# Kernel tuning notes

Measured on AMD Instinct MI355X. Metric: run time of the kernel, lower is better.

## Reference

```python
import jax, jax.numpy as jnp
import numpy as np

N, E = 50000, 800000
DIN, DOUT, DIM, K = 64, 64, 3, 8
EPS_GMM = 1e-15
BN_EPS = 1e-5
ALPHA = 0.01


def setup_inputs() -> dict:
    key = jax.random.key(0)
    ks = jax.random.split(key, 10)
    x = jax.random.normal(ks[0], (N, DIN), dtype=jnp.float32)
    edge_idx = jax.random.randint(ks[1], (2, E), 0, N, dtype=jnp.int64)
    edge_attr = jax.random.uniform(ks[2], (E, DIM), dtype=jnp.float32)
    # GMMConv params (PyG: g maps in -> K*out, lin is root weight, plus bias)
    W_g = jax.random.normal(ks[3], (DIN, K * DOUT), dtype=jnp.float32) * (1.0 / np.sqrt(DIN))
    mu = jax.random.normal(ks[4], (K, DIM), dtype=jnp.float32)
    sigma = jnp.ones((K, DIM), dtype=jnp.float32) + 0.1 * jax.random.normal(ks[5], (K, DIM), dtype=jnp.float32)
    W_root = jax.random.normal(ks[6], (DIN, DOUT), dtype=jnp.float32) * (1.0 / np.sqrt(DIN))
    bias = jnp.zeros((DOUT,), dtype=jnp.float32)
    gamma = jnp.ones((DOUT,), dtype=jnp.float32)
    beta = jnp.zeros((DOUT,), dtype=jnp.float32)
    return {"x": x, "edge_idx": edge_idx, "edge_attr": edge_attr,
            "W_g": W_g, "mu": mu, "sigma": sigma, "W_root": W_root,
            "bias": bias, "gamma": gamma, "beta": beta}


def reference(x, edge_idx, edge_attr, W_g, mu, sigma, W_root, bias, gamma, beta):
    src, dst = edge_idx[0], edge_idx[1]
    # Gaussian mixture edge weights: [E, K]
    diff = edge_attr[:, None, :] - mu[None, :, :]              # [E, K, DIM]
    gauss = jnp.exp((-0.5 * diff * diff / (EPS_GMM + sigma[None] ** 2)).sum(-1))  # [E, K]
    # Transform node features once: [N, K, DOUT]
    x_trans = (x @ W_g).reshape(N, K, DOUT)
    # Per-edge message: weighted sum over kernels of gathered source features
    msg = jnp.einsum('ekm,ek->em', x_trans[src], gauss)        # [E, DOUT]
    # Mean-aggregate to destination nodes
    agg = jax.ops.segment_sum(msg, dst, num_segments=N)        # [N, DOUT]
    cnt = jax.ops.segment_sum(jnp.ones((E,), dtype=x.dtype), dst, num_segments=N)
    agg = agg / jnp.maximum(cnt, 1.0)[:, None]
    # Root weight + bias
    out = agg + x @ W_root + bias
    # BatchNorm1d (training mode: batch stats, biased variance)
    m = out.mean(axis=0)
    v = ((out - m) ** 2).mean(axis=0)
    out = gamma * (out - m) * jax.lax.rsqrt(v + BN_EPS) + beta
    # LeakyReLU
    return jnp.where(out > 0, out, ALPHA * out)
```

## Files before the change

kernel.cpp:

```cpp
#include <hip/hip_runtime.h>
#include <hip/hip_bf16.h>

#define N_NODES 50000
#define N_EDGES 800000
#define NB 391
#define BCAP 2560

typedef __hip_bfloat16 bf16;

__device__ __forceinline__ float bf_lo(int u) { union { int i; float f; } c; c.i = (unsigned)u << 16; return c.f; }
__device__ __forceinline__ float bf_hi(int u) { union { int i; float f; } c; c.i = (unsigned)u & 0xffff0000u; return c.f; }
__device__ __forceinline__ unsigned short bfbits(float f) {
    bf16 b = __float2bfloat16(f);
    union { bf16 b; unsigned short u; } c; c.b = b; return c.u;
}

__global__ void gemm_xt_kernel(const float* __restrict__ x, const float* __restrict__ Wg,
                               bf16* __restrict__ xt) {
    __shared__ float xs[16][64];
    __shared__ float lb[16 * 512];
    const int tid = threadIdx.x;
    const int row0 = blockIdx.x << 4;
    for (int i = tid; i < 1024; i += 256) xs[i >> 6][i & 63] = x[(size_t)row0 * 64 + i];
    __syncthreads();

    float a0[16], a1[16];
#pragma unroll
    for (int r = 0; r < 16; r++) { a0[r] = 0.f; a1[r] = 0.f; }
#pragma unroll 4
    for (int i = 0; i < 64; i++) {
        const float w0 = Wg[i * 512 + tid];
        const float w1 = Wg[i * 512 + tid + 256];
#pragma unroll
        for (int r = 0; r < 16; r++) {
            const float xv = xs[r][i];
            a0[r] = fmaf(xv, w0, a0[r]);
            a1[r] = fmaf(xv, w1, a1[r]);
        }
    }
#pragma unroll
    for (int r = 0; r < 16; r++) {
        lb[r * 512 + tid] = a0[r];
        lb[r * 512 + tid + 256] = a1[r];
    }
    __syncthreads();

    const int m = tid & 63, rg = tid >> 6;
#pragma unroll
    for (int rr = 0; rr < 4; rr++) {
        const int r = rg * 4 + rr;
        unsigned short h[8];
#pragma unroll
        for (int k = 0; k < 8; k++) h[k] = bfbits(lb[r * 512 + k * 64 + m]);
        int4 q;
        q.x = (int)h[0] | ((int)h[1] << 16);
        q.y = (int)h[2] | ((int)h[3] << 16);
        q.z = (int)h[4] | ((int)h[5] << 16);
        q.w = (int)h[6] | ((int)h[7] << 16);
        ((int4*)(xt + (size_t)(row0 + r) * 512))[m] = q;
    }
}

__global__ void __launch_bounds__(1024) scatter_kernel(const int* __restrict__ eidx,
                                                       const float* __restrict__ eattr,
                                                       const float* __restrict__ mu,
                                                       const float* __restrict__ sigma,
                                                       int* __restrict__ cursor,
                                                       unsigned* __restrict__ meta,
                                                       int4* __restrict__ g8v) {
    __shared__ float smu[24], sc1[24];
    __shared__ int cnt[NB], base[NB];
    const int tid = threadIdx.x;
    if (tid < 24) {
        smu[tid] = mu[tid];
        const float s = sigma[tid];
        sc1[tid] = -0.5f / (s * s + 1e-15f);
    }
    if (tid < NB) cnt[tid] = 0;
    __syncthreads();

    const int e = blockIdx.x * 1024 + tid;
    const bool act = e < N_EDGES;
    int b = 0, rank = 0;
    unsigned mt = 0;
    int4 q = {0, 0, 0, 0};
    if (act) {
        const int src = eidx[e];
        const int dst = eidx[N_EDGES + e];
        const float A0 = eattr[3 * e + 0];
        const float A1 = eattr[3 * e + 1];
        const float A2 = eattr[3 * e + 2];
        unsigned short h[8];
#pragma unroll
        for (int k = 0; k < 8; k++) {
            const float d0 = A0 - smu[3 * k + 0];
            const float d1 = A1 - smu[3 * k + 1];
            const float d2 = A2 - smu[3 * k + 2];
            const float g = __expf(fmaf(d0 * d0, sc1[3 * k + 0],
                                   fmaf(d1 * d1, sc1[3 * k + 1],
                                        d2 * d2 * sc1[3 * k + 2])));
            h[k] = bfbits(g);
        }
        q.x = (int)h[0] | ((int)h[1] << 16);
        q.y = (int)h[2] | ((int)h[3] << 16);
        q.z = (int)h[4] | ((int)h[5] << 16);
        q.w = (int)h[6] | ((int)h[7] << 16);
        b = dst >> 7;
        mt = (unsigned)src | ((unsigned)(dst & 127) << 16);
        rank = atomicAdd(&cnt[b], 1);
    }
    __syncthreads();
    if (tid < NB) {
        const int c = cnt[tid];
        base[tid] = c ? atomicAdd(&cursor[tid], c) : 0;
    }
    __syncthreads();
    if (act) {
        const int slot = b * BCAP + base[b] + rank;
        meta[slot] = mt;
        g8v[slot] = q;
    }
}

__global__ void __launch_bounds__(1024) agg_kernel(const int* __restrict__ cursor,
                                                   const unsigned* __restrict__ meta,
                                                   const int4* __restrict__ g8v,
                                                   const bf16* __restrict__ xt,
                                                   const float* __restrict__ x,
                                                   const float* __restrict__ Wr,
                                                   const float* __restrict__ bias,
                                                   float* __restrict__ out,
                                                   double* __restrict__ colsum,
                                                   double* __restrict__ colsumsq) {
    __shared__ float acc[128 * 64];
    __shared__ float wr[4096];
    __shared__ int cnt[128];
    __shared__ float red[16 * 64];

    const int tid = threadIdx.x;
    const int b = blockIdx.x;
    for (int i = tid; i < 8192; i += 1024) acc[i] = 0.f;
    if (tid < 128) cnt[tid] = 0;
    for (int i = tid; i < 4096; i += 1024) wr[i] = Wr[i];
    __syncthreads();

    int count = cursor[b];
    if (count > BCAP) count = BCAP;
    const int wid = tid >> 6, lane = tid & 63;
    const int baseSlot = b * BCAP;

    for (int j = wid; j < count; j += 16) {
        const unsigned mt = meta[baseSlot + j];
        const int4 g = g8v[baseSlot + j];
        const int src = mt & 0xffff;
        const int dl = (mt >> 16) & 127;
        const int4 qx = *(const int4*)(xt + (size_t)src * 512 + lane * 8);
        const float v = bf_lo(g.x) * bf_lo(qx.x) + bf_hi(g.x) * bf_hi(qx.x)
                      + bf_lo(g.y) * bf_lo(qx.y) + bf_hi(g.y) * bf_hi(qx.y)
                      + bf_lo(g.z) * bf_lo(qx.z) + bf_hi(g.z) * bf_hi(qx.z)
                      + bf_lo(g.w) * bf_lo(qx.w) + bf_hi(g.w) * bf_hi(qx.w);
        atomicAdd(&acc[dl * 64 + lane], v);
        if (lane == 0) atomicAdd(&cnt[dl], 1);
    }
    __syncthreads();

    const float bsv = bias[lane];
    float s = 0.f, sq = 0.f;
#pragma unroll
    for (int t = 0; t < 8; t++) {
        const int nl = wid * 8 + t;
        const int n = b * 128 + nl;
        if (n < N_NODES) {
            const float* xr = x + (size_t)n * 64;
            float a = 0.f;
#pragma unroll
            for (int i = 0; i < 64; i++) a = fmaf(xr[i], wr[i * 64 + lane], a);
            const float c = (float)cnt[nl];
            const float val = acc[nl * 64 + lane] / fmaxf(c, 1.f) + a + bsv;
            out[(size_t)n * 64 + lane] = val;
            s += val;
            sq += val * val;
        }
    }
    red[wid * 64 + lane] = s;
    __syncthreads();
    float ts = 0.f;
    if (wid == 0) {
#pragma unroll
        for (int w = 0; w < 16; w++) ts += red[w * 64 + lane];
    }
    __syncthreads();
    red[wid * 64 + lane] = sq;
    __syncthreads();
    if (wid == 0) {
        float tq = 0.f;
#pragma unroll
        for (int w = 0; w < 16; w++) tq += red[w * 64 + lane];
        atomicAdd(&colsum[lane], (double)ts);
        atomicAdd(&colsumsq[lane], (double)tq);
    }
}

__global__ void bn_prep_kernel(const double* __restrict__ colsum, const double* __restrict__ colsumsq,
                               float* __restrict__ meanr) {
    const int c = threadIdx.x;
    if (c < 64) {
        const double m = colsum[c] / (double)N_NODES;
        const double var = colsumsq[c] / (double)N_NODES - m * m;
        meanr[c] = (float)m;
        meanr[64 + c] = (float)(1.0 / sqrt(var + 1e-5));
    }
}

__global__ void finalize_kernel(float* __restrict__ out, const float* __restrict__ meanr,
                                const float* __restrict__ gamma, const float* __restrict__ beta) {
    const int i = blockIdx.x * 256 + threadIdx.x;
    const int c = i & 63;
    const float v = out[i];
    const float o = fmaf((v - meanr[c]) * meanr[64 + c], gamma[c], beta[c]);
    out[i] = o > 0.f ? o : 0.01f * o;
}

extern "C" void kernel_launch(void* const* d_in, const int* in_sizes, int n_in,
                              void* d_out, int out_size, void* d_ws, size_t ws_size,
                              hipStream_t stream) {
    const float* x     = (const float*)d_in[0];
    const int*   eidx  = (const int*)d_in[1];
    const float* eattr = (const float*)d_in[2];
    const float* Wg    = (const float*)d_in[3];
    const float* mu    = (const float*)d_in[4];
    const float* sigma = (const float*)d_in[5];
    const float* Wr    = (const float*)d_in[6];
    const float* bias  = (const float*)d_in[7];
    const float* gamma = (const float*)d_in[8];
    const float* beta  = (const float*)d_in[9];
    float* out = (float*)d_out;

    char* ws = (char*)d_ws;
    const size_t cursor_off   = 0;
    const size_t colsum_off   = 2048;
    const size_t colsumsq_off = 2560;
    const size_t zero_bytes   = 3072;
    const size_t meanr_off    = 3072;
    const size_t meta_off     = 3584;
    const size_t g8_off       = 4017664;
    const size_t xt_off       = 20073984;

    int*      cursor   = (int*)(ws + cursor_off);
    double*   colsum   = (double*)(ws + colsum_off);
    double*   colsumsq = (double*)(ws + colsumsq_off);
    float*    meanr    = (float*)(ws + meanr_off);
    unsigned* meta     = (unsigned*)(ws + meta_off);
    int4*     g8v      = (int4*)(ws + g8_off);
    bf16*     xt       = (bf16*)(ws + xt_off);

    hipMemsetAsync(ws, 0, zero_bytes, stream);
    gemm_xt_kernel<<<N_NODES / 16, 256, 0, stream>>>(x, Wg, xt);
    scatter_kernel<<<(N_EDGES + 1023) / 1024, 1024, 0, stream>>>(eidx, eattr, mu, sigma, cursor, meta, g8v);
    agg_kernel<<<NB, 1024, 0, stream>>>(cursor, meta, g8v, xt, x, Wr, bias, out, colsum, colsumsq);
    bn_prep_kernel<<<1, 64, 0, stream>>>(colsum, colsumsq, meanr);
    finalize_kernel<<<(N_NODES * 64) / 256, 256, 0, stream>>>(out, meanr, gamma, beta);
}
```

Before: 587.6 us.

## Use smaller 32-node destination buckets with batched gathers in aggregation

Destination buckets shrink from 128 to 32 nodes, so there are 1563 aggregation blocks of 256 threads in place of 391 blocks of 1024, giving better load spread across CUs. Each wave now loads 64 edge metadata entries at once and broadcasts them by shuffle, issuing four independent source-row gathers before accumulating. The root-weight matmul stages x rows in shared memory and reads Wr from global/cache in place of a shared copy. Bucket capacity drops to 704 with an overflow guard, which risks silently dropping edges if any bucket receives more.

```diff
diff --git a/kernel.cpp b/kernel.cpp
--- a/kernel.cpp
+++ b/kernel.cpp
@@ -3,8 +3,8 @@
 
 #define N_NODES 50000
 #define N_EDGES 800000
-#define NB 391
-#define BCAP 2560
+#define NB 1563
+#define BCAP 704
 
 typedef __hip_bfloat16 bf16;
 
@@ -13,6 +13,12 @@
 __device__ __forceinline__ unsigned short bfbits(float f) {
     bf16 b = __float2bfloat16(f);
     union { bf16 b; unsigned short u; } c; c.b = b; return c.u;
+}
+__device__ __forceinline__ float dot8(const int4 g, const int4 qx) {
+    return bf_lo(g.x) * bf_lo(qx.x) + bf_hi(g.x) * bf_hi(qx.x)
+         + bf_lo(g.y) * bf_lo(qx.y) + bf_hi(g.y) * bf_hi(qx.y)
+         + bf_lo(g.z) * bf_lo(qx.z) + bf_hi(g.z) * bf_hi(qx.z)
+         + bf_lo(g.w) * bf_lo(qx.w) + bf_hi(g.w) * bf_hi(qx.w);
 }
 
 __global__ void gemm_xt_kernel(const float* __restrict__ x, const float* __restrict__ Wg,
@@ -76,7 +82,7 @@
         const float s = sigma[tid];
         sc1[tid] = -0.5f / (s * s + 1e-15f);
     }
-    if (tid < NB) cnt[tid] = 0;
+    for (int i = tid; i < NB; i += 1024) cnt[i] = 0;
     __syncthreads();
 
     const int e = blockIdx.x * 1024 + tid;
@@ -105,62 +111,86 @@
         q.y = (int)h[2] | ((int)h[3] << 16);
         q.z = (int)h[4] | ((int)h[5] << 16);
         q.w = (int)h[6] | ((int)h[7] << 16);
-        b = dst >> 7;
-        mt = (unsigned)src | ((unsigned)(dst & 127) << 16);
+        b = dst >> 5;
+        mt = (unsigned)src | ((unsigned)(dst & 31) << 16);
         rank = atomicAdd(&cnt[b], 1);
     }
     __syncthreads();
-    if (tid < NB) {
-        const int c = cnt[tid];
-        base[tid] = c ? atomicAdd(&cursor[tid], c) : 0;
+    for (int i = tid; i < NB; i += 1024) {
+        const int c = cnt[i];
+        base[i] = c ? atomicAdd(&cursor[i], c) : 0;
     }
     __syncthreads();
     if (act) {
         const int slot = b * BCAP + base[b] + rank;
-        meta[slot] = mt;
-        g8v[slot] = q;
-    }
-}
-
-__global__ void __launch_bounds__(1024) agg_kernel(const int* __restrict__ cursor,
-                                                   const unsigned* __restrict__ meta,
-                                                   const int4* __restrict__ g8v,
-                                                   const bf16* __restrict__ xt,
-                                                   const float* __restrict__ x,
-                                                   const float* __restrict__ Wr,
-                                                   const float* __restrict__ bias,
-                                                   float* __restrict__ out,
-                                                   double* __restrict__ colsum,
-                                                   double* __restrict__ colsumsq) {
-    __shared__ float acc[128 * 64];
-    __shared__ float wr[4096];
-    __shared__ int cnt[128];
-    __shared__ float red[16 * 64];
+        if (slot < (b + 1) * BCAP) {
+            meta[slot] = mt;
+            g8v[slot] = q;
+        }
+    }
+}
+
+__global__ void __launch_bounds__(256) agg_kernel(const int* __restrict__ cursor,
+                                                  const unsigned* __restrict__ meta,
+                                                  const int4* __restrict__ g8v,
+                                                  const bf16* __restrict__ xt,
+                                                  const float* __restrict__ x,
+                                                  const float* __restrict__ Wr,
+                                                  const float* __restrict__ bias,
+                                                  float* __restrict__ out,
+                                                  double* __restrict__ colsum,
+                                                  double* __restrict__ colsumsq) {
+    __shared__ float acc[32 * 64];
+    __shared__ float xs[32 * 64];
+    __shared__ int cnt_s[32];
+    __shared__ float red[4 * 64];
 
     const int tid = threadIdx.x;
     const int b = blockIdx.x;
-    for (int i = tid; i < 8192; i += 1024) acc[i] = 0.f;
-    if (tid < 128) cnt[tid] = 0;
-    for (int i = tid; i < 4096; i += 1024) wr[i] = Wr[i];
+    for (int i = tid; i < 2048; i += 256) acc[i] = 0.f;
+    if (tid < 32) cnt_s[tid] = 0;
     __syncthreads();
 
     int count = cursor[b];
     if (count > BCAP) count = BCAP;
     const int wid = tid >> 6, lane = tid & 63;
-    const int baseSlot = b * BCAP;
-
-    for (int j = wid; j < count; j += 16) {
-        const unsigned mt = meta[baseSlot + j];
-        const int4 g = g8v[baseSlot + j];
-        const int src = mt & 0xffff;
-        const int dl = (mt >> 16) & 127;
-        const int4 qx = *(const int4*)(xt + (size_t)src * 512 + lane * 8);
-        const float v = bf_lo(g.x) * bf_lo(qx.x) + bf_hi(g.x) * bf_hi(qx.x)
-                      + bf_lo(g.y) * bf_lo(qx.y) + bf_hi(g.y) * bf_hi(qx.y)
-                      + bf_lo(g.z) * bf_lo(qx.z) + bf_hi(g.z) * bf_hi(qx.z)
-                      + bf_lo(g.w) * bf_lo(qx.w) + bf_hi(g.w) * bf_hi(qx.w);
-        atomicAdd(&acc[dl * 64 + lane], v);
-        if (lane == 0) atomicAdd(&cnt[dl], 1);
+    const int bbase = b * BCAP;
+
+    for (int jc = wid * 64; jc < count; jc += 256) {
+        const int nv = min(64, count - jc);
+        unsigned mt = 0;
+        if (lane < nv) mt = meta[bbase + jc + lane];
+
+        int u = 0;
+        for (; u + 4 <= nv; u += 4) {
+            int4 qx[4];
+            int dls[4];
+#pragma unroll
+            for (int t = 0; t < 4; t++) {
+                const unsigned m = (unsigned)__shfl((int)mt, u + t, 64);
+                qx[t] = *(const int4*)(xt + (size_t)(m & 0xffffu) * 512 + lane * 8);
+                dls[t] = (m >> 16) & 31;
+            }
+#pragma unroll
+            for (int t = 0; t < 4; t++) {
+                const int4 g = g8v[bbase + jc + u + t];
+                atomicAdd(&acc[dls[t] * 64 + lane], dot8(g, qx[t]));
+                if (lane == 0) atomicAdd(&cnt_s[dls[t]], 1);
+            }
+        }
+        for (; u < nv; u++) {
+            const unsigned m = (unsigned)__shfl((int)mt, u, 64);
+            const int4 qx = *(const int4*)(xt + (size_t)(m & 0xffffu) * 512 + lane * 8);
+            const int dl = (m >> 16) & 31;
+            const int4 g = g8v[bbase + jc + u];
+            atomicAdd(&acc[dl * 64 + lane], dot8(g, qx));
+            if (lane == 0) atomicAdd(&cnt_s[dl], 1);
+        }
+    }
+
+    for (int i = tid; i < 2048; i += 256) {
+        const int n = b * 32 + (i >> 6);
+        xs[i] = (n < N_NODES) ? x[(size_t)n * 64 + (i & 63)] : 0.f;
     }
     __syncthreads();
 
@@ -169,13 +199,12 @@
 #pragma unroll
     for (int t = 0; t < 8; t++) {
         const int nl = wid * 8 + t;
-        const int n = b * 128 + nl;
+        const int n = b * 32 + nl;
         if (n < N_NODES) {
-            const float* xr = x + (size_t)n * 64;
             float a = 0.f;
 #pragma unroll
-            for (int i = 0; i < 64; i++) a = fmaf(xr[i], wr[i * 64 + lane], a);
-            const float c = (float)cnt[nl];
+            for (int i = 0; i < 64; i++) a = fmaf(xs[nl * 64 + i], Wr[i * 64 + lane], a);
+            const float c = (float)cnt_s[nl];
             const float val = acc[nl * 64 + lane] / fmaxf(c, 1.f) + a + bsv;
             out[(size_t)n * 64 + lane] = val;
             s += val;
@@ -185,17 +214,12 @@
     red[wid * 64 + lane] = s;
     __syncthreads();
     float ts = 0.f;
+    if (wid == 0) ts = red[lane] + red[64 + lane] + red[128 + lane] + red[192 + lane];
+    __syncthreads();
+    red[wid * 64 + lane] = sq;
+    __syncthreads();
     if (wid == 0) {
-#pragma unroll
-        for (int w = 0; w < 16; w++) ts += red[w * 64 + lane];
-    }
-    __syncthreads();
-    red[wid * 64 + lane] = sq;
-    __syncthreads();
-    if (wid == 0) {
-        float tq = 0.f;
-#pragma unroll
-        for (int w = 0; w < 16; w++) tq += red[w * 64 + lane];
+        const float tq = red[lane] + red[64 + lane] + red[128 + lane] + red[192 + lane];
         atomicAdd(&colsum[lane], (double)ts);
         atomicAdd(&colsumsq[lane], (double)tq);
     }
@@ -238,13 +262,13 @@
 
     char* ws = (char*)d_ws;
     const size_t cursor_off   = 0;
-    const size_t colsum_off   = 2048;
-    const size_t colsumsq_off = 2560;
-    const size_t zero_bytes   = 3072;
-    const size_t meanr_off    = 3072;
-    const size_t meta_off     = 3584;
-    const size_t g8_off       = 4017664;
-    const size_t xt_off       = 20073984;
+    const size_t colsum_off   = 6400;
+    const size_t colsumsq_off = 6912;
+    const size_t zero_bytes   = 7424;
+    const size_t meanr_off    = 7424;
+    const size_t meta_off     = 7936;
+    const size_t g8_off       = 4409344;
+    const size_t xt_off       = 22014976;
 
     int*      cursor   = (int*)(ws + cursor_off);
     double*   colsum   = (double*)(ws + colsum_off);
@@ -257,7 +281,7 @@
     hipMemsetAsync(ws, 0, zero_bytes, stream);
     gemm_xt_kernel<<<N_NODES / 16, 256, 0, stream>>>(x, Wg, xt);
     scatter_kernel<<<(N_EDGES + 1023) / 1024, 1024, 0, stream>>>(eidx, eattr, mu, sigma, cursor, meta, g8v);
-    agg_kernel<<<NB, 1024, 0, stream>>>(cursor, meta, g8v, xt, x, Wr, bias, out, colsum, colsumsq);
+    agg_kernel<<<NB, 256, 0, stream>>>(cursor, meta, g8v, xt, x, Wr, bias, out, colsum, colsumsq);
     bn_prep_kernel<<<1, 64, 0, stream>>>(colsum, colsumsq, meanr);
     finalize_kernel<<<(N_NODES * 64) / 256, 256, 0, stream>>>(out, meanr, gamma, beta);
 }
```

Result: faster. 524.9 us (-10.7%).

## Aggregate gauss-weighted raw features per node before applying W_g

Applied to the files above, without the earlier changes.

Reorders the math so each node first accumulates per-kernel gaussian-weighted sums of bf16 source features, then applies W_g once per node, instead of gathering the precomputed 512-wide transformed features per edge. This removes the big N×512 GEMM and cuts per-edge gather traffic from 1KB to 128B. Edges are bucketed into 4-node bins with two scatter passes so the shared-memory bin counters fit. One wave handles each bin and accumulates in registers, with no shared-memory atomics. Bins are capped at 128 edges and overflow is silently dropped, which risks wrong results on skewed degree. The per-node W_g matmul now uses shuffles and repeated global weight loads.

```diff
diff --git a/kernel.cpp b/kernel.cpp
--- a/kernel.cpp
+++ b/kernel.cpp
@@ -3,62 +3,24 @@
 
 #define N_NODES 50000
 #define N_EDGES 800000
-#define NB 391
-#define BCAP 2560
+#define NSB 12500
+#define BCAP 128
+#define SCAT_BINS 6250
 
 typedef __hip_bfloat16 bf16;
 
-__device__ __forceinline__ float bf_lo(int u) { union { int i; float f; } c; c.i = (unsigned)u << 16; return c.f; }
-__device__ __forceinline__ float bf_hi(int u) { union { int i; float f; } c; c.i = (unsigned)u & 0xffff0000u; return c.f; }
-__device__ __forceinline__ unsigned short bfbits(float f) {
-    bf16 b = __float2bfloat16(f);
-    union { bf16 b; unsigned short u; } c; c.b = b; return c.u;
-}
-
-__global__ void gemm_xt_kernel(const float* __restrict__ x, const float* __restrict__ Wg,
-                               bf16* __restrict__ xt) {
-    __shared__ float xs[16][64];
-    __shared__ float lb[16 * 512];
-    const int tid = threadIdx.x;
-    const int row0 = blockIdx.x << 4;
-    for (int i = tid; i < 1024; i += 256) xs[i >> 6][i & 63] = x[(size_t)row0 * 64 + i];
-    __syncthreads();
-
-    float a0[16], a1[16];
-#pragma unroll
-    for (int r = 0; r < 16; r++) { a0[r] = 0.f; a1[r] = 0.f; }
-#pragma unroll 4
-    for (int i = 0; i < 64; i++) {
-        const float w0 = Wg[i * 512 + tid];
-        const float w1 = Wg[i * 512 + tid + 256];
-#pragma unroll
-        for (int r = 0; r < 16; r++) {
-            const float xv = xs[r][i];
-            a0[r] = fmaf(xv, w0, a0[r]);
-            a1[r] = fmaf(xv, w1, a1[r]);
-        }
-    }
-#pragma unroll
-    for (int r = 0; r < 16; r++) {
-        lb[r * 512 + tid] = a0[r];
-        lb[r * 512 + tid + 256] = a1[r];
-    }
-    __syncthreads();
-
-    const int m = tid & 63, rg = tid >> 6;
-#pragma unroll
-    for (int rr = 0; rr < 4; rr++) {
-        const int r = rg * 4 + rr;
-        unsigned short h[8];
-#pragma unroll
-        for (int k = 0; k < 8; k++) h[k] = bfbits(lb[r * 512 + k * 64 + m]);
-        int4 q;
-        q.x = (int)h[0] | ((int)h[1] << 16);
-        q.y = (int)h[2] | ((int)h[3] << 16);
-        q.z = (int)h[4] | ((int)h[5] << 16);
-        q.w = (int)h[6] | ((int)h[7] << 16);
-        ((int4*)(xt + (size_t)(row0 + r) * 512))[m] = q;
-    }
+__device__ __forceinline__ float bf_lo(int u){ union{unsigned i;float f;}c; c.i=(unsigned)u<<16; return c.f; }
+__device__ __forceinline__ float bf_hi(int u){ union{unsigned i;float f;}c; c.i=(unsigned)u&0xffff0000u; return c.f; }
+__device__ __forceinline__ unsigned short bfbits(float f){
+    bf16 b=__float2bfloat16(f); union{bf16 b;unsigned short u;}c; c.b=b; return c.u;
+}
+__device__ __forceinline__ float us2f(unsigned short u){ union{unsigned i;float f;}c; c.i=(unsigned)u<<16; return c.f; }
+
+__global__ void cast_x_kernel(const float* __restrict__ x, unsigned short* __restrict__ xb){
+    const int i = blockIdx.x*256 + threadIdx.x;
+    const float4 v = ((const float4*)x)[i];
+    ushort4 o; o.x=bfbits(v.x); o.y=bfbits(v.y); o.z=bfbits(v.z); o.w=bfbits(v.w);
+    ((ushort4*)xb)[i] = o;
 }
 
 __global__ void __launch_bounds__(1024) scatter_kernel(const int* __restrict__ eidx,
@@ -67,163 +29,208 @@
                                                        const float* __restrict__ sigma,
                                                        int* __restrict__ cursor,
                                                        unsigned* __restrict__ meta,
-                                                       int4* __restrict__ g8v) {
+                                                       int4* __restrict__ g8v,
+                                                       int b0){
     __shared__ float smu[24], sc1[24];
-    __shared__ int cnt[NB], base[NB];
+    __shared__ int cnt[SCAT_BINS], bbase[SCAT_BINS];
     const int tid = threadIdx.x;
-    if (tid < 24) {
+    if (tid < 24){
         smu[tid] = mu[tid];
         const float s = sigma[tid];
-        sc1[tid] = -0.5f / (s * s + 1e-15f);
-    }
-    if (tid < NB) cnt[tid] = 0;
-    __syncthreads();
-
-    const int e = blockIdx.x * 1024 + tid;
-    const bool act = e < N_EDGES;
-    int b = 0, rank = 0;
-    unsigned mt = 0;
-    int4 q = {0, 0, 0, 0};
-    if (act) {
+        sc1[tid] = -0.5f/(s*s + 1e-15f);
+    }
+    for (int i=tid;i<SCAT_BINS;i+=1024) cnt[i]=0;
+    __syncthreads();
+
+    const int e = blockIdx.x*1024 + tid;
+    bool act=false; int b=0, rank=0, dst=0;
+    unsigned mt=0; int4 q={0,0,0,0};
+    if (e < N_EDGES){
+        dst = eidx[N_EDGES + e];
+        b = (dst>>2) - b0;
+        act = (b>=0) && (b<SCAT_BINS);
+    }
+    if (act){
         const int src = eidx[e];
-        const int dst = eidx[N_EDGES + e];
-        const float A0 = eattr[3 * e + 0];
-        const float A1 = eattr[3 * e + 1];
-        const float A2 = eattr[3 * e + 2];
+        const float A0 = eattr[3*e+0];
+        const float A1 = eattr[3*e+1];
+        const float A2 = eattr[3*e+2];
         unsigned short h[8];
 #pragma unroll
-        for (int k = 0; k < 8; k++) {
-            const float d0 = A0 - smu[3 * k + 0];
-            const float d1 = A1 - smu[3 * k + 1];
-            const float d2 = A2 - smu[3 * k + 2];
-            const float g = __expf(fmaf(d0 * d0, sc1[3 * k + 0],
-                                   fmaf(d1 * d1, sc1[3 * k + 1],
-                                        d2 * d2 * sc1[3 * k + 2])));
+        for (int k=0;k<8;k++){
+            const float d0 = A0 - smu[3*k+0];
+            const float d1 = A1 - smu[3*k+1];
+            const float d2 = A2 - smu[3*k+2];
+            const float g = __expf(fmaf(d0*d0, sc1[3*k+0],
+                               fmaf(d1*d1, sc1[3*k+1], d2*d2*sc1[3*k+2])));
             h[k] = bfbits(g);
         }
-        q.x = (int)h[0] | ((int)h[1] << 16);
-        q.y = (int)h[2] | ((int)h[3] << 16);
-        q.z = (int)h[4] | ((int)h[5] << 16);
-        q.w = (int)h[6] | ((int)h[7] << 16);
-        b = dst >> 7;
-        mt = (unsigned)src | ((unsigned)(dst & 127) << 16);
+        q.x = (int)h[0]|((int)h[1]<<16);
+        q.y = (int)h[2]|((int)h[3]<<16);
+        q.z = (int)h[4]|((int)h[5]<<16);
+        q.w = (int)h[6]|((int)h[7]<<16);
+        mt = (unsigned)src | ((unsigned)(dst&3)<<16);
         rank = atomicAdd(&cnt[b], 1);
     }
     __syncthreads();
-    if (tid < NB) {
-        const int c = cnt[tid];
-        base[tid] = c ? atomicAdd(&cursor[tid], c) : 0;
-    }
-    __syncthreads();
-    if (act) {
-        const int slot = b * BCAP + base[b] + rank;
-        meta[slot] = mt;
-        g8v[slot] = q;
-    }
-}
-
-__global__ void __launch_bounds__(1024) agg_kernel(const int* __restrict__ cursor,
-                                                   const unsigned* __restrict__ meta,
-                                                   const int4* __restrict__ g8v,
-                                                   const bf16* __restrict__ xt,
-                                                   const float* __restrict__ x,
-                                                   const float* __restrict__ Wr,
-                                                   const float* __restrict__ bias,
-                                                   float* __restrict__ out,
-                                                   double* __restrict__ colsum,
-                                                   double* __restrict__ colsumsq) {
-    __shared__ float acc[128 * 64];
-    __shared__ float wr[4096];
-    __shared__ int cnt[128];
-    __shared__ float red[16 * 64];
-
-    const int tid = threadIdx.x;
-    const int b = blockIdx.x;
-    for (int i = tid; i < 8192; i += 1024) acc[i] = 0.f;
-    if (tid < 128) cnt[tid] = 0;
-    for (int i = tid; i < 4096; i += 1024) wr[i] = Wr[i];
-    __syncthreads();
-
-    int count = cursor[b];
-    if (count > BCAP) count = BCAP;
-    const int wid = tid >> 6, lane = tid & 63;
-    const int baseSlot = b * BCAP;
-
-    for (int j = wid; j < count; j += 16) {
-        const unsigned mt = meta[baseSlot + j];
-        const int4 g = g8v[baseSlot + j];
-        const int src = mt & 0xffff;
-        const int dl = (mt >> 16) & 127;
-        const int4 qx = *(const int4*)(xt + (size_t)src * 512 + lane * 8);
-        const float v = bf_lo(g.x) * bf_lo(qx.x) + bf_hi(g.x) * bf_hi(qx.x)
-                      + bf_lo(g.y) * bf_lo(qx.y) + bf_hi(g.y) * bf_hi(qx.y)
-                      + bf_lo(g.z) * bf_lo(qx.z) + bf_hi(g.z) * bf_hi(qx.z)
-                      + bf_lo(g.w) * bf_lo(qx.w) + bf_hi(g.w) * bf_hi(qx.w);
-        atomicAdd(&acc[dl * 64 + lane], v);
-        if (lane == 0) atomicAdd(&cnt[dl], 1);
-    }
-    __syncthreads();
-
-    const float bsv = bias[lane];
-    float s = 0.f, sq = 0.f;
-#pragma unroll
-    for (int t = 0; t < 8; t++) {
-        const int nl = wid * 8 + t;
-        const int n = b * 128 + nl;
-        if (n < N_NODES) {
-            const float* xr = x + (size_t)n * 64;
-            float a = 0.f;
-#pragma unroll
-            for (int i = 0; i < 64; i++) a = fmaf(xr[i], wr[i * 64 + lane], a);
-            const float c = (float)cnt[nl];
-            const float val = acc[nl * 64 + lane] / fmaxf(c, 1.f) + a + bsv;
-            out[(size_t)n * 64 + lane] = val;
-            s += val;
-            sq += val * val;
-        }
-    }
-    red[wid * 64 + lane] = s;
-    __syncthreads();
+    for (int i=tid;i<SCAT_BINS;i+=1024){
+        const int c = cnt[i];
+        if (c) bbase[i] = atomicAdd(&cursor[b0+i], c);
+    }
+    __syncthreads();
+    if (act){
+        const int pos = bbase[b] + rank;
+        if (pos < BCAP){
+            const int slot = (b0+b)*BCAP + pos;
+            meta[slot] = mt;
+            g8v[slot] = q;
+        }
+    }
+}
+
+__global__ void __launch_bounds__(256, 4) agg_kernel(const int* __restrict__ cursor,
+                                                     const unsigned* __restrict__ meta,
+                                                     const int4* __restrict__ g8v,
+                                                     const unsigned short* __restrict__ xb,
+                                                     const float* __restrict__ x,
+                                                     const float* __restrict__ Wg,
+                                                     const float* __restrict__ Wr,
+                                                     const float* __restrict__ bias,
+                                                     float* __restrict__ out,
+                                                     double* __restrict__ colsum,
+                                                     double* __restrict__ colsumsq){
+    __shared__ float red[256];
+    const int tid = threadIdx.x, w = tid>>6, lane = tid&63;
+    const int sb = blockIdx.x*4 + w;
+    int count = cursor[sb]; if (count > BCAP) count = BCAP;
+    const int base = sb*BCAP;
+
+    float acc[4][8];
+#pragma unroll
+    for (int j=0;j<4;j++)
+#pragma unroll
+        for (int k=0;k<8;k++) acc[j][k]=0.f;
+    int cnt0=0,cnt1=0,cnt2=0,cnt3=0;
+
+#define ACC8(J,CNT) { CNT++; \
+    acc[J][0]=fmaf(bf_lo(gq.x),xv,acc[J][0]); acc[J][1]=fmaf(bf_hi(gq.x),xv,acc[J][1]); \
+    acc[J][2]=fmaf(bf_lo(gq.y),xv,acc[J][2]); acc[J][3]=fmaf(bf_hi(gq.y),xv,acc[J][3]); \
+    acc[J][4]=fmaf(bf_lo(gq.z),xv,acc[J][4]); acc[J][5]=fmaf(bf_hi(gq.z),xv,acc[J][5]); \
+    acc[J][6]=fmaf(bf_lo(gq.w),xv,acc[J][6]); acc[J][7]=fmaf(bf_hi(gq.w),xv,acc[J][7]); }
+
+    for (int jc=0; jc<count; jc+=64){
+        const int nv = min(64, count-jc);
+        unsigned mt = 0;
+        if (lane < nv) mt = meta[base+jc+lane];
+        int u = 0;
+        for (; u+4<=nv; u+=4){
+            unsigned mm[4]; unsigned short raw[4];
+#pragma unroll
+            for (int t=0;t<4;t++) mm[t] = (unsigned)__shfl((int)mt, u+t, 64);
+#pragma unroll
+            for (int t=0;t<4;t++) raw[t] = xb[(int)(mm[t]&0xffffu)*64 + lane];
+#pragma unroll
+            for (int t=0;t<4;t++){
+                const int4 gq = g8v[base+jc+u+t];
+                const float xv = us2f(raw[t]);
+                switch ((mm[t]>>16)&3){
+                    case 0: ACC8(0,cnt0); break;
+                    case 1: ACC8(1,cnt1); break;
+                    case 2: ACC8(2,cnt2); break;
+                    default: ACC8(3,cnt3); break;
+                }
+            }
+        }
+        for (; u<nv; u++){
+            const unsigned m = (unsigned)__shfl((int)mt, u, 64);
+            const int4 gq = g8v[base+jc+u];
+            const float xv = us2f(xb[(int)(m&0xffffu)*64 + lane]);
+            switch ((m>>16)&3){
+                case 0: ACC8(0,cnt0); break;
+                case 1: ACC8(1,cnt1); break;
+                case 2: ACC8(2,cnt2); break;
+                default: ACC8(3,cnt3); break;
+            }
+        }
+    }
+
+    float c0=0.f,c1=0.f,c2=0.f,c3=0.f;
+#pragma unroll
+    for (int k=0;k<8;k++){
+#pragma unroll 4
+        for (int d=0;d<64;d++){
+            const float wv = Wg[d*512 + k*64 + lane];
+            c0 = fmaf(__shfl(acc[0][k], d, 64), wv, c0);
+            c1 = fmaf(__shfl(acc[1][k], d, 64), wv, c1);
+            c2 = fmaf(__shfl(acc[2][k], d, 64), wv, c2);
+            c3 = fmaf(__shfl(acc[3][k], d, 64), wv, c3);
+        }
+    }
+
+    const int n0 = blockIdx.x*16 + w*4;
+    const float xv0 = x[(n0+0)*64 + lane];
+    const float xv1 = x[(n0+1)*64 + lane];
+    const float xv2 = x[(n0+2)*64 + lane];
+    const float xv3 = x[(n0+3)*64 + lane];
+    float r0=0.f,r1=0.f,r2=0.f,r3=0.f;
+#pragma unroll 4
+    for (int i=0;i<64;i++){
+        const float wrv = Wr[i*64 + lane];
+        r0 = fmaf(__shfl(xv0,i,64), wrv, r0);
+        r1 = fmaf(__shfl(xv1,i,64), wrv, r1);
+        r2 = fmaf(__shfl(xv2,i,64), wrv, r2);
+        r3 = fmaf(__shfl(xv3,i,64), wrv, r3);
+    }
+
+    const float bv = bias[lane];
+    float s=0.f, sq=0.f;
+    {
+        const float v0 = c0/fmaxf((float)cnt0,1.f) + r0 + bv;
+        out[(n0+0)*64+lane] = v0; s += v0; sq += v0*v0;
+        const float v1 = c1/fmaxf((float)cnt1,1.f) + r1 + bv;
+        out[(n0+1)*64+lane] = v1; s += v1; sq += v1*v1;
+        const float v2 = c2/fmaxf((float)cnt2,1.f) + r2 + bv;
+        out[(n0+2)*64+lane] = v2; s += v2; sq += v2*v2;
+        const float v3 = c3/fmaxf((float)cnt3,1.f) + r3 + bv;
+        out[(n0+3)*64+lane] = v3; s += v3; sq += v3*v3;
+    }
+
+    red[tid] = s; __syncthreads();
     float ts = 0.f;
-    if (wid == 0) {
-#pragma unroll
-        for (int w = 0; w < 16; w++) ts += red[w * 64 + lane];
-    }
-    __syncthreads();
-    red[wid * 64 + lane] = sq;
-    __syncthreads();
-    if (wid == 0) {
-        float tq = 0.f;
-#pragma unroll
-        for (int w = 0; w < 16; w++) tq += red[w * 64 + lane];
+    if (w==0) ts = red[lane]+red[64+lane]+red[128+lane]+red[192+lane];
+    __syncthreads();
+    red[tid] = sq; __syncthreads();
+    if (w==0){
+        const float tq = red[lane]+red[64+lane]+red[128+lane]+red[192+lane];
         atomicAdd(&colsum[lane], (double)ts);
         atomicAdd(&colsumsq[lane], (double)tq);
     }
+#undef ACC8
 }
 
 __global__ void bn_prep_kernel(const double* __restrict__ colsum, const double* __restrict__ colsumsq,
-                               float* __restrict__ meanr) {
+                               float* __restrict__ meanr){
     const int c = threadIdx.x;
-    if (c < 64) {
-        const double m = colsum[c] / (double)N_NODES;
-        const double var = colsumsq[c] / (double)N_NODES - m * m;
+    if (c < 64){
+        const double m = colsum[c]/(double)N_NODES;
+        const double var = colsumsq[c]/(double)N_NODES - m*m;
         meanr[c] = (float)m;
-        meanr[64 + c] = (float)(1.0 / sqrt(var + 1e-5));
+        meanr[64+c] = (float)(1.0/sqrt(var + 1e-5));
     }
 }
 
 __global__ void finalize_kernel(float* __restrict__ out, const float* __restrict__ meanr,
-                                const float* __restrict__ gamma, const float* __restrict__ beta) {
-    const int i = blockIdx.x * 256 + threadIdx.x;
+                                const float* __restrict__ gamma, const float* __restrict__ beta){
+    const int i = blockIdx.x*256 + threadIdx.x;
     const int c = i & 63;
     const float v = out[i];
-    const float o = fmaf((v - meanr[c]) * meanr[64 + c], gamma[c], beta[c]);
-    out[i] = o > 0.f ? o : 0.01f * o;
+    const float o = fmaf((v - meanr[c])*meanr[64+c], gamma[c], beta[c]);
+    out[i] = o > 0.f ? o : 0.01f*o;
 }
 
 extern "C" void kernel_launch(void* const* d_in, const int* in_sizes, int n_in,
                               void* d_out, int out_size, void* d_ws, size_t ws_size,
-                              hipStream_t stream) {
+                              hipStream_t stream){
     const float* x     = (const float*)d_in[0];
     const int*   eidx  = (const int*)d_in[1];
     const float* eattr = (const float*)d_in[2];
@@ -238,26 +245,27 @@
 
     char* ws = (char*)d_ws;
     const size_t cursor_off   = 0;
-    const size_t colsum_off   = 2048;
-    const size_t colsumsq_off = 2560;
-    const size_t zero_bytes   = 3072;
-    const size_t meanr_off    = 3072;
-    const size_t meta_off     = 3584;
-    const size_t g8_off       = 4017664;
-    const size_t xt_off       = 20073984;
-
-    int*      cursor   = (int*)(ws + cursor_off);
-    double*   colsum   = (double*)(ws + colsum_off);
-    double*   colsumsq = (double*)(ws + colsumsq_off);
-    float*    meanr    = (float*)(ws + meanr_off);
-    unsigned* meta     = (unsigned*)(ws + meta_off);
-    int4*     g8v      = (int4*)(ws + g8_off);
-    bf16*     xt       = (bf16*)(ws + xt_off);
+    const size_t colsum_off   = 50176;
+    const size_t colsumsq_off = 50688;
+    const size_t zero_bytes   = 51200;
+    const size_t meanr_off    = 51200;
+    const size_t meta_off     = 51712;
+    const size_t g8_off       = 6451712;
+    const size_t xb_off       = 32051712;
+
+    int*            cursor   = (int*)(ws + cursor_off);
+    double*         colsum   = (double*)(ws + colsum_off);
+    double*         colsumsq = (double*)(ws + colsumsq_off);
+    float*          meanr    = (float*)(ws + meanr_off);
+    unsigned*       meta     = (unsigned*)(ws + meta_off);
+    int4*           g8v      = (int4*)(ws + g8_off);
+    unsigned short* xb       = (unsigned short*)(ws + xb_off);
 
     hipMemsetAsync(ws, 0, zero_bytes, stream);
-    gemm_xt_kernel<<<N_NODES / 16, 256, 0, stream>>>(x, Wg, xt);
-    scatter_kernel<<<(N_EDGES + 1023) / 1024, 1024, 0, stream>>>(eidx, eattr, mu, sigma, cursor, meta, g8v);
-    agg_kernel<<<NB, 1024, 0, stream>>>(cursor, meta, g8v, xt, x, Wr, bias, out, colsum, colsumsq);
+    cast_x_kernel<<<3125, 256, 0, stream>>>(x, xb);
+    scatter_kernel<<<(N_EDGES + 1023)/1024, 1024, 0, stream>>>(eidx, eattr, mu, sigma, cursor, meta, g8v, 0);
+    scatter_kernel<<<(N_EDGES + 1023)/1024, 1024, 0, stream>>>(eidx, eattr, mu, sigma, cursor, meta, g8v, SCAT_BINS);
+    agg_kernel<<<NSB/4, 256, 0, stream>>>(cursor, meta, g8v, xb, x, Wg, Wr, bias, out, colsum, colsumsq);
     bn_prep_kernel<<<1, 64, 0, stream>>>(colsum, colsumsq, meanr);
-    finalize_kernel<<<(N_NODES * 64) / 256, 256, 0, stream>>>(out, meanr, gamma, beta);
-}
+    finalize_kernel<<<(N_NODES*64)/256, 256, 0, stream>>>(out, meanr, gamma, beta);
+}
```

New measurement: 511.7 us. -12.9%, faster.
